# Optimization experiments

Measured on AMD Instinct MI355X. Metric: run time of the kernel, lower is better.

## Reference

```python
import jax, jax.numpy as jnp
import numpy as np

B, S, D_IN, E, H = 2, 2048, 1024, 1024, 16  # batch, seq, input_size, embedding_size, heads


def setup_inputs() -> dict:
    key = jax.random.key(0)
    k1, k2, k3 = jax.random.split(key, 3)
    x = jax.random.normal(k1, (B, S, D_IN), dtype=jnp.float32)
    # fused QKV projection weight stored as [in, 3E] (torch Linear weight transposed)
    W0 = jax.random.normal(k2, (D_IN, 3 * E), dtype=jnp.float32) * (1.0 / np.sqrt(D_IN))
    b0 = jax.random.normal(k3, (3 * E,), dtype=jnp.float32) * 0.02
    return {"x": x, "W0": W0, "b0": b0}


def reference(x, W0, b0):
    b, s, _ = x.shape
    y = x @ W0 + b0                              # [B,S,3E]
    y = y.reshape(b, s, H, -1).transpose(0, 2, 1, 3)  # [B,H,S,3*head_dim]
    q, k, v = jnp.split(y, 3, axis=-1)           # each [B,H,S,head_dim]
    scale = 1.0 / jnp.sqrt(jnp.asarray(D_IN, dtype=x.dtype))  # NB: sqrt(input_size), as in source
    scores = jnp.einsum("bhqd,bhkd->bhqk", q, k) * scale
    # causal mask: -inf above diagonal
    causal = jnp.triu(jnp.full((s, s), -jnp.inf, dtype=scores.dtype), k=1)
    scores = scores + causal
    attn = jax.nn.softmax(scores, axis=-1)       # [B,H,S,S]
    o = jnp.einsum("bhqk,bhkd->bhqd", attn, v)   # [B,H,S,head_dim]
    # faithful to source: reshape directly from (B,H,S,d) to (B,S,H*d) WITHOUT permuting back
    return o.reshape(b, s, -1)
```

## Files before the change

### kernel.cpp

```cpp
#include <hip/hip_runtime.h>
#include <stdint.h>

typedef __attribute__((ext_vector_type(4))) float f32x4;
typedef __attribute__((ext_vector_type(16))) float f32x16;
typedef __attribute__((ext_vector_type(8))) short bf16x8;
typedef __attribute__((ext_vector_type(4))) short bf16x4;

#define MFMA16(a, b, c) __builtin_amdgcn_mfma_f32_16x16x32_bf16((a), (b), (c), 0, 0, 0)
#define MFMA32(a, b, c) __builtin_amdgcn_mfma_f32_32x32x16_bf16((a), (b), (c), 0, 0, 0)

__device__ __forceinline__ short f2bf(float f) {
    union { float f; uint32_t u; } v; v.f = f;
    uint32_t r = (v.u + 0x7fffu + ((v.u >> 16) & 1u)) >> 16;
    return (short)(uint16_t)r;
}
__device__ __forceinline__ float bf2f(short s) {
    union { uint32_t u; float f; } v; v.u = ((uint32_t)(uint16_t)s) << 16;
    return v.f;
}
__device__ __forceinline__ float fast_exp2(float x) {
    float r; asm("v_exp_f32 %0, %1" : "=v"(r) : "v"(x)); return r;
}

__device__ __forceinline__ void async_ld16(const short* g, short* l) {
    __builtin_amdgcn_global_load_lds(
        (const __attribute__((address_space(1))) uint32_t*)g,
        (__attribute__((address_space(3))) uint32_t*)l, 16, 0, 0);
}

#define MK_BFRAG(C, O, OUT) do {                                                   \
    uint32_t a_, b_, c_, d_;                                                       \
    asm("v_cvt_pk_bf16_f32 %0, %1, %2" : "=v"(a_) : "v"((C)[(O)+0]), "v"((C)[(O)+1])); \
    asm("v_cvt_pk_bf16_f32 %0, %1, %2" : "=v"(c_) : "v"((C)[(O)+2]), "v"((C)[(O)+3])); \
    asm("v_cvt_pk_bf16_f32 %0, %1, %2" : "=v"(b_) : "v"((C)[(O)+4]), "v"((C)[(O)+5])); \
    asm("v_cvt_pk_bf16_f32 %0, %1, %2" : "=v"(d_) : "v"((C)[(O)+6]), "v"((C)[(O)+7])); \
    asm("v_permlane32_swap_b32 %0, %1" : "+v"(a_), "+v"(b_));                      \
    asm("v_permlane32_swap_b32 %0, %1" : "+v"(c_), "+v"(d_));                      \
    union { uint32_t u[4]; bf16x8 v; } pb_;                                        \
    pb_.u[0] = a_; pb_.u[1] = c_; pb_.u[2] = b_; pb_.u[3] = d_;                    \
    OUT = pb_.v;                                                                   \
} while (0)

__global__ __launch_bounds__(256)
void convert_fused(const float* __restrict__ X, short* __restrict__ Xb,
                   const float* __restrict__ W, short* __restrict__ Wt) {
    __shared__ short T[64][72];
    const int t = threadIdx.x;
    const int id = blockIdx.x;
    if (id < 2048) {
        const int i8 = (id * 256 + t) << 3;
        f32x4 a = *(const f32x4*)(X + i8);
        f32x4 b = *(const f32x4*)(X + i8 + 4);
        bf16x8 o;
#pragma unroll
        for (int j = 0; j < 4; ++j) { o[j] = f2bf(a[j]); o[4 + j] = f2bf(b[j]); }
        *(bf16x8*)(Xb + i8) = o;
        return;
    }
    const int wid = id - 2048;
    const int n0 = (wid % 48) * 64, k0 = (wid / 48) * 64;
#pragma unroll
    for (int i = 0; i < 4; ++i) {
        const int r = i * 16 + (t >> 4);
        const int c = (t & 15) << 2;
        f32x4 v = *(const f32x4*)(W + (size_t)(k0 + r) * 3072 + n0 + c);
#pragma unroll
        for (int j = 0; j < 4; ++j) T[c + j][r] = f2bf(v[j]);
    }
    __syncthreads();
#pragma unroll
    for (int i = 0; i < 2; ++i) {
        const int r = i * 32 + (t >> 3);
        const int c = (t & 7) << 3;
        *(bf16x8*)(Wt + (size_t)(n0 + r) * 1024 + k0 + c) = *(const bf16x8*)&T[r][c];
    }
}

__global__ __launch_bounds__(256, 3)
void gemm_pack(const short* __restrict__ Xb, const short* __restrict__ Wt,
               const float* __restrict__ bias, short* __restrict__ Qp,
               short* __restrict__ Kp, short* __restrict__ Vp) {
    __shared__ short Asm[2][128 * 32];
    __shared__ short Bsm[2][128 * 32];

    const int tid  = threadIdx.x;
    const int lane = tid & 63;
    const int l15  = lane & 15;
    const int lq   = lane >> 4;
    const int wave = tid >> 6;
    const int wr = wave >> 1, wc = wave & 1;

    const int bid = blockIdx.x;
    const int swz = (bid & 7) * 96 + (bid >> 3);
    const int m0 = (swz / 24) * 128, n0 = (swz % 24) * 128;

    const int srow = tid >> 2;
    const int scolsw = (((tid & 3) ^ ((srow >> 1) & 3)) << 3);

    f32x4 acc[4][4];
#pragma unroll
    for (int m = 0; m < 4; ++m)
#pragma unroll
        for (int n = 0; n < 4; ++n) acc[m][n] = (f32x4)(0.0f);

    auto stage = [&](int k0, int bb) {
#pragma unroll
        for (int i = 0; i < 2; ++i)
            async_ld16(Xb + (size_t)(m0 + i * 64 + srow) * 1024 + k0 + scolsw,
                       &Asm[bb][(i * 256 + wave * 64) * 8]);
#pragma unroll
        for (int i = 0; i < 2; ++i)
            async_ld16(Wt + (size_t)(n0 + i * 64 + srow) * 1024 + k0 + scolsw,
                       &Bsm[bb][(i * 256 + wave * 64) * 8]);
    };

    const int gsw = ((lq ^ ((l15 >> 1) & 3)) << 3);

    auto compute = [&](int bb) {
        bf16x8 af[4], bfv[4];
#pragma unroll
        for (int m = 0; m < 4; ++m)
            af[m] = *(const bf16x8*)&Asm[bb][(wr * 64 + m * 16 + l15) * 32 + gsw];
#pragma unroll
        for (int n = 0; n < 4; ++n)
            bfv[n] = *(const bf16x8*)&Bsm[bb][(wc * 64 + n * 16 + l15) * 32 + gsw];
#pragma unroll
        for (int m = 0; m < 4; ++m)
#pragma unroll
            for (int n = 0; n < 4; ++n) acc[m][n] = MFMA16(af[m], bfv[n], acc[m][n]);
    };

    stage(0, 0);
#pragma unroll 1
    for (int kt = 0; kt < 32; ++kt) {
        if (kt < 31) {
            stage((kt + 1) * 32, (kt + 1) & 1);
            asm volatile("s_waitcnt vmcnt(4)" ::: "memory");
        } else {
            asm volatile("s_waitcnt vmcnt(0)" ::: "memory");
        }
        __builtin_amdgcn_sched_barrier(0);
        __builtin_amdgcn_s_barrier();
        __builtin_amdgcn_sched_barrier(0);
        compute(kt & 1);
        __builtin_amdgcn_sched_barrier(0);
        __builtin_amdgcn_s_barrier();
        __builtin_amdgcn_sched_barrier(0);
    }

    const float SCALE2 = 0.03125f * 1.44269504f;
    float bv[4];
#pragma unroll
    for (int n = 0; n < 4; ++n) bv[n] = bias[n0 + wc * 64 + n * 16 + l15];

    const size_t bbase = (size_t)(m0 >> 11) * 2097152;
    const int tokb = (m0 & 2047) + wr * 64;

#pragma unroll
    for (int n = 0; n < 4; ++n) {
        const int col = n0 + wc * 64 + n * 16 + l15;
        const int h   = col / 192;
        const int seg = (col >> 6) % 3;
        const int d   = col & 63;
        const size_t hb = bbase + (size_t)h * 131072;
        if (seg == 0) {
            const int cp = ((d >> 4) << 9) + (((d >> 3) & 1) << 8) + (d & 7);
#pragma unroll
            for (int m = 0; m < 4; ++m)
#pragma unroll
                for (int r = 0; r < 4; ++r) {
                    const int tok = tokb + m * 16 + (lq << 2) + r;
                    Qp[hb + ((size_t)(tok >> 5) << 11) + ((tok & 31) << 3) + cp] =
                        f2bf((acc[m][n][r] + bv[n]) * SCALE2);
                }
        } else if (seg == 1) {
            const int cp = ((d >> 4) << 10) + (((d >> 3) & 1) << 8) + (d & 7);
#pragma unroll
            for (int m = 0; m < 4; ++m)
#pragma unroll
                for (int r = 0; r < 4; ++r) {
                    const int tok = tokb + m * 16 + (lq << 2) + r;
                    Kp[hb + ((size_t)(tok >> 6) << 12) + (((tok >> 5) & 1) << 9)
                       + ((tok & 31) << 3) + cp] = f2bf(acc[m][n][r] + bv[n]);
                }
        } else {
            const int cp = ((d >> 5) << 11) + ((d & 31) << 3);
#pragma unroll
            for (int m = 0; m < 4; ++m)
#pragma unroll
                for (int r = 0; r < 4; ++r) {
                    const int tok = tokb + m * 16 + (lq << 2) + r;
                    Vp[hb + ((size_t)(tok >> 6) << 12) + (((tok >> 4) & 3) << 9)
                       + (((tok >> 3) & 1) << 8) + (tok & 7) + cp] =
                        f2bf(acc[m][n][r] + bv[n]);
                }
        }
    }
}

__global__ __launch_bounds__(64, 2)
void attn_part(const short* __restrict__ Qp, const short* __restrict__ Kp,
               const short* __restrict__ Vp, short* __restrict__ Po,
               float* __restrict__ Pm) {
    const int tid = threadIdx.x;
    const int l31 = tid & 31;
    const int hi  = tid >> 5;

    const int id  = blockIdx.x;
    const int xcd = id & 7;
    const int idx = id >> 3;
    const int u   = idx >> 2;
    const int bh  = xcd * 4 + (idx & 3);

    int qt, t0, t1;
    bool hasDiag;
    if (u < 32) {
        qt = u + 32; t0 = 0; t1 = 16; hasDiag = false;
    } else {
        const int s = 16 - ((u - 32) >> 2);
        const int j = (u - 32) & 3;
        if (j < 2) { qt = 2 * s - 2 + j;       t0 = 0;  t1 = s; }
        else       { qt = 2 * s + 30 + (j - 2); t0 = 16; t1 = s + 16; }
        hasDiag = true;
    }
    const int q0 = qt * 32;

    const size_t hb = (size_t)bh * 131072;

    bf16x8 qf[4];
    {
        const short* qp = Qp + hb + qt * 2048 + tid * 8;
#pragma unroll
        for (int dg = 0; dg < 4; ++dg) qf[dg] = *(const bf16x8*)(qp + dg * 512);
    }

    f32x16 o0 = (f32x16)(0.f), o1 = (f32x16)(0.f);
    float m_run = -1e30f, l_run = 0.f;
    const int qg = q0 + l31;

    bf16x8 kA[8], kB[8], va[8];

    auto loadK = [&](bf16x8 (&kr)[8], int t) {
        const short* p = Kp + hb + (size_t)t * 4096 + tid * 8;
#pragma unroll
        for (int f = 0; f < 8; ++f)
            kr[f] = *(const bf16x8*)(p + (f >> 1) * 1024 + (f & 1) * 512);
    };
    auto loadV = [&](int t) {
        const short* p = Vp + hb + (size_t)t * 4096 + tid * 8;
#pragma unroll
        for (int f = 0; f < 8; ++f) va[f] = *(const bf16x8*)(p + f * 512);
    };
    auto qk = [&](bf16x8 (&kr)[8], f32x16& c0, f32x16& c1) {
#pragma unroll
        for (int dg = 0; dg < 4; ++dg) {
            c0 = MFMA32(kr[2 * dg],     qf[dg], c0);
            c1 = MFMA32(kr[2 * dg + 1], qf[dg], c1);
        }
    };

    auto smpv = [&](f32x16& c0, f32x16& c1, int kv0, bool DIAG) {
        if (DIAG) {
#pragma unroll
            for (int r = 0; r < 16; ++r) {
                const int kvr = kv0 + (r & 3) + 8 * (r >> 2) + 4 * hi;
                if (kvr > qg)      c0[r] = -1e30f;
                if (kvr + 32 > qg) c1[r] = -1e30f;
            }
        }

        float mr[8];
#pragma unroll
        for (int r = 0; r < 8; ++r)
            mr[r] = fmaxf(fmaxf(c0[r], c0[8 + r]), fmaxf(c1[r], c1[8 + r]));
        float mx = fmaxf(fmaxf(fmaxf(mr[0], mr[1]), fmaxf(mr[2], mr[3])),
                         fmaxf(fmaxf(mr[4], mr[5]), fmaxf(mr[6], mr[7])));
        mx = fmaxf(mx, __shfl_xor(mx, 32, 64));

        if (!__all(mx <= m_run + 8.f)) {
            const float mnew = fmaxf(m_run, mx);
            const float corr = fast_exp2(m_run - mnew);
            l_run *= corr;
            o0 = o0 * corr;
            o1 = o1 * corr;
            m_run = mnew;
        }

        float ps0 = 0.f, ps1 = 0.f, ps2 = 0.f, ps3 = 0.f;
#pragma unroll
        for (int r = 0; r < 4; ++r) {
            c0[r]      = fast_exp2(c0[r]      - m_run); ps0 += c0[r];
            c0[4 + r]  = fast_exp2(c0[4 + r]  - m_run); ps1 += c0[4 + r];
            c0[8 + r]  = fast_exp2(c0[8 + r]  - m_run); ps2 += c0[8 + r];
            c0[12 + r] = fast_exp2(c0[12 + r] - m_run); ps3 += c0[12 + r];
        }
#pragma unroll
        for (int r = 0; r < 4; ++r) {
            c1[r]      = fast_exp2(c1[r]      - m_run); ps0 += c1[r];
            c1[4 + r]  = fast_exp2(c1[4 + r]  - m_run); ps1 += c1[4 + r];
            c1[8 + r]  = fast_exp2(c1[8 + r]  - m_run); ps2 += c1[8 + r];
            c1[12 + r] = fast_exp2(c1[12 + r] - m_run); ps3 += c1[12 + r];
        }
        l_run += (ps0 + ps1) + (ps2 + ps3);

        bf16x8 bf00, bf01, bf10, bf11;
        MK_BFRAG(c0, 0, bf00);
        MK_BFRAG(c0, 8, bf01);
        MK_BFRAG(c1, 0, bf10);
        MK_BFRAG(c1, 8, bf11);

        o0 = MFMA32(va[0], bf00, o0);
        o0 = MFMA32(va[1], bf01, o0);
        o0 = MFMA32(va[2], bf10, o0);
        o0 = MFMA32(va[3], bf11, o0);
        o1 = MFMA32(va[4], bf00, o1);
        o1 = MFMA32(va[5], bf01, o1);
        o1 = MFMA32(va[6], bf10, o1);
        o1 = MFMA32(va[7], bf11, o1);
    };

    int t = t0;
    loadK(kA, t0);
#pragma unroll 1
    for (; t + 2 < t1; t += 2) {
        f32x16 c0 = (f32x16)(0.f), c1 = (f32x16)(0.f);
        qk(kA, c0, c1);
        loadK(kB, t + 1);
        loadV(t);
        smpv(c0, c1, t * 64, false);
        f32x16 d0 = (f32x16)(0.f), d1 = (f32x16)(0.f);
        qk(kB, d0, d1);
        loadK(kA, t + 2);
        loadV(t + 1);
        smpv(d0, d1, (t + 1) * 64, false);
    }
    if (t + 1 < t1) {
        f32x16 c0 = (f32x16)(0.f), c1 = (f32x16)(0.f);
        qk(kA, c0, c1);
        loadK(kB, t + 1);
        loadV(t);
        smpv(c0, c1, t * 64, false);
        f32x16 d0 = (f32x16)(0.f), d1 = (f32x16)(0.f);
        qk(kB, d0, d1);
        loadV(t + 1);
        smpv(d0, d1, (t + 1) * 64, hasDiag);
    } else {
        f32x16 c0 = (f32x16)(0.f), c1 = (f32x16)(0.f);
        qk(kA, c0, c1);
        loadV(t);
        smpv(c0, c1, t * 64, hasDiag);
    }

    const float l_tot = l_run + __shfl_xor(l_run, 32, 64);
    const float inv = 1.f / l_tot;
    const int prow = (bh * 96 + u) * 32 + l31;
#pragma unroll
    for (int g = 0; g < 4; ++g) {
        bf16x4 w4;
#pragma unroll
        for (int j = 0; j < 4; ++j) w4[j] = f2bf(o0[g * 4 + j] * inv);
        *(bf16x4*)&Po[(size_t)prow * 64 + 8 * g + 4 * hi] = w4;
#pragma unroll
        for (int j = 0; j < 4; ++j) w4[j] = f2bf(o1[g * 4 + j] * inv);
        *(bf16x4*)&Po[(size_t)prow * 64 + 32 + 4 * hi + 8 * g] = w4;
    }
    if (hi == 0) Pm[prow] = m_run + __log2f(l_tot);
}

__global__ __launch_bounds__(256)
void attn_combine(const short* __restrict__ Po, const float* __restrict__ Pm,
                  float* __restrict__ Out) {
    const int idx = blockIdx.x * 256 + threadIdx.x;
    const int d4 = (idx & 15) << 2;
    const int rg = idx >> 4;
    const int q  = rg & 2047;
    const int bh = rg >> 11;
    const int qt = q >> 5, r = q & 31;

    f32x4 ov;
    if (qt < 32) {
        const int s = (qt >> 1) + 1;
        const int u = 32 + (16 - s) * 4 + (qt & 1);
        const int p0 = (bh * 96 + u) * 32 + r;
        bf16x4 a = *(const bf16x4*)&Po[(size_t)p0 * 64 + d4];
#pragma unroll
        for (int j = 0; j < 4; ++j) ov[j] = bf2f(a[j]);
    } else {
        const int u0 = qt - 32;
        const int s  = (qt >> 1) - 15;
        const int u1 = 32 + (16 - s) * 4 + 2 + (qt & 1);
        const int p0 = (bh * 96 + u0) * 32 + r;
        const int p1 = (bh * 96 + u1) * 32 + r;
        bf16x4 a = *(const bf16x4*)&Po[(size_t)p0 * 64 + d4];
        bf16x4 c = *(const bf16x4*)&Po[(size_t)p1 * 64 + d4];
        const float m0 = Pm[p0], m1 = Pm[p1];
        const float M = fmaxf(m0, m1);
        const float w0 = exp2f(m0 - M), w1 = exp2f(m1 - M);
        const float inv = 1.f / (w0 + w1);
#pragma unroll
        for (int j = 0; j < 4; ++j) ov[j] = (w0 * bf2f(a[j]) + w1 * bf2f(c[j])) * inv;
    }
    *(f32x4*)&Out[(size_t)rg * 64 + d4] = ov;
}

extern "C" void kernel_launch(void* const* d_in, const int* in_sizes, int n_in,
                              void* d_out, int out_size, void* d_ws, size_t ws_size,
                              hipStream_t stream) {
    const float* x  = (const float*)d_in[0];
    const float* W0 = (const float*)d_in[1];
    const float* b0 = (const float*)d_in[2];
    float* out = (float*)d_out;
    char* ws = (char*)d_ws;

    const size_t SEG_B = (size_t)32 * 131072 * 2;
    const size_t QKV_B = 3 * SEG_B;
    const size_t XBF_B = (size_t)4096 * 1024 * 2;
    const size_t PO_B  = (size_t)32 * 96 * 32 * 64 * 2;

    short* qp = (short*)ws;
    short* kp = (short*)(ws + SEG_B);
    short* vp = (short*)(ws + 2 * SEG_B);
    short* xb = (short*)(ws + QKV_B);
    short* wt = (short*)(ws + QKV_B + XBF_B);
    short* po = (short*)(ws + QKV_B);
    float* pm = (float*)(ws + QKV_B + PO_B);

    convert_fused<<<dim3(2816), dim3(256), 0, stream>>>(x, xb, W0, wt);
    gemm_pack<<<dim3(768), dim3(256), 0, stream>>>(xb, wt, b0, qp, kp, vp);
    attn_part<<<dim3(3072), dim3(64), 0, stream>>>(qp, kp, vp, po, pm);
    attn_combine<<<dim3(4096), dim3(256), 0, stream>>>(po, pm, out);
}
```

Baseline: 84.31 us.

## Double GEMM K-tile to 64 with new XOR-swizzled LDS layout

The QKV projection GEMM now stages 64-wide K slices instead of 32, halving the number of main-loop iterations and barrier pairs. The LDS staging pattern and XOR swizzle are reworked for 64-element rows, and each compute step issues two MFMAs per accumulator. The cost is twice the shared memory per block, so launch bounds drop from 3 to 2 blocks per CU, which may reduce latency hiding.

```diff
diff --git a/kernel.cpp b/kernel.cpp
--- a/kernel.cpp
+++ b/kernel.cpp
@@ -76,12 +76,12 @@
     }
 }
 
-__global__ __launch_bounds__(256, 3)
+__global__ __launch_bounds__(256, 2)
 void gemm_pack(const short* __restrict__ Xb, const short* __restrict__ Wt,
                const float* __restrict__ bias, short* __restrict__ Qp,
                short* __restrict__ Kp, short* __restrict__ Vp) {
-    __shared__ short Asm[2][128 * 32];
-    __shared__ short Bsm[2][128 * 32];
+    __shared__ short Asm[2][128 * 64];
+    __shared__ short Bsm[2][128 * 64];
 
     const int tid  = threadIdx.x;
     const int lane = tid & 63;
@@ -94,8 +94,9 @@
     const int swz = (bid & 7) * 96 + (bid >> 3);
     const int m0 = (swz / 24) * 128, n0 = (swz % 24) * 128;
 
-    const int srow = tid >> 2;
-    const int scolsw = (((tid & 3) ^ ((srow >> 1) & 3)) << 3);
+    const int r8 = lane >> 3;
+    const int s8 = lane & 7;
+    const int scolsw = ((s8 ^ r8) << 3);
 
     f32x4 acc[4][4];
 #pragma unroll
@@ -105,37 +106,47 @@
 
     auto stage = [&](int k0, int bb) {
 #pragma unroll
-        for (int i = 0; i < 2; ++i)
-            async_ld16(Xb + (size_t)(m0 + i * 64 + srow) * 1024 + k0 + scolsw,
-                       &Asm[bb][(i * 256 + wave * 64) * 8]);
-#pragma unroll
-        for (int i = 0; i < 2; ++i)
-            async_ld16(Wt + (size_t)(n0 + i * 64 + srow) * 1024 + k0 + scolsw,
-                       &Bsm[bb][(i * 256 + wave * 64) * 8]);
-    };
-
-    const int gsw = ((lq ^ ((l15 >> 1) & 3)) << 3);
+        for (int i = 0; i < 4; ++i)
+            async_ld16(Xb + (size_t)(m0 + i * 32 + wave * 8 + r8) * 1024 + k0 + scolsw,
+                       &Asm[bb][(i * 32 + wave * 8) * 64]);
+#pragma unroll
+        for (int i = 0; i < 4; ++i)
+            async_ld16(Wt + (size_t)(n0 + i * 32 + wave * 8 + r8) * 1024 + k0 + scolsw,
+                       &Bsm[bb][(i * 32 + wave * 8) * 64]);
+    };
+
+    const int sl0 = ((lq ^ (l15 & 7)) << 3);
+    const int sl1 = (((4 + lq) ^ (l15 & 7)) << 3);
 
     auto compute = [&](int bb) {
-        bf16x8 af[4], bfv[4];
+        bf16x8 afA[4], afB[4], bfA[4], bfB[4];
+#pragma unroll
+        for (int m = 0; m < 4; ++m) {
+            const int rb = (wr * 64 + m * 16 + l15) * 64;
+            afA[m] = *(const bf16x8*)&Asm[bb][rb + sl0];
+            afB[m] = *(const bf16x8*)&Asm[bb][rb + sl1];
+        }
+#pragma unroll
+        for (int n = 0; n < 4; ++n) {
+            const int rb = (wc * 64 + n * 16 + l15) * 64;
+            bfA[n] = *(const bf16x8*)&Bsm[bb][rb + sl0];
+            bfB[n] = *(const bf16x8*)&Bsm[bb][rb + sl1];
+        }
 #pragma unroll
         for (int m = 0; m < 4; ++m)
-            af[m] = *(const bf16x8*)&Asm[bb][(wr * 64 + m * 16 + l15) * 32 + gsw];
-#pragma unroll
-        for (int n = 0; n < 4; ++n)
-            bfv[n] = *(const bf16x8*)&Bsm[bb][(wc * 64 + n * 16 + l15) * 32 + gsw];
-#pragma unroll
-        for (int m = 0; m < 4; ++m)
-#pragma unroll
-            for (int n = 0; n < 4; ++n) acc[m][n] = MFMA16(af[m], bfv[n], acc[m][n]);
+#pragma unroll
+            for (int n = 0; n < 4; ++n) {
+                acc[m][n] = MFMA16(afA[m], bfA[n], acc[m][n]);
+                acc[m][n] = MFMA16(afB[m], bfB[n], acc[m][n]);
+            }
     };
 
     stage(0, 0);
 #pragma unroll 1
-    for (int kt = 0; kt < 32; ++kt) {
-        if (kt < 31) {
-            stage((kt + 1) * 32, (kt + 1) & 1);
-            asm volatile("s_waitcnt vmcnt(4)" ::: "memory");
+    for (int kt = 0; kt < 16; ++kt) {
+        if (kt < 15) {
+            stage((kt + 1) * 64, (kt + 1) & 1);
+            asm volatile("s_waitcnt vmcnt(8)" ::: "memory");
         } else {
             asm volatile("s_waitcnt vmcnt(0)" ::: "memory");
         }
```

Result: slower. 88.68 us (+5.2%).
